# Performance work log

Hardware: AMD Instinct MI355X
Metric: run time of the kernel (lower is better)

Reference implementation:

```python
import jax, jax.numpy as jnp
import numpy as np

L_V, L_T, D, H, HID = 1024, 128, 4096, 8, 2048
N1 = L_V // 2      # tokens kept by selector module 1
N2 = N1 // 2       # tokens kept by selector module 2 (final selected)
N_REM = L_V - N2   # remaining tokens to merge


def setup_inputs() -> dict:
    key = jax.random.key(0)
    ks = jax.random.split(key, 8)
    s = 0.02
    return {
        "vision_feature": jax.random.normal(ks[0], (L_V, D), jnp.float32),
        "text_embed": jax.random.normal(ks[1], (L_T, D), jnp.float32),
        "attention_mask": jnp.ones((L_T,), jnp.int32),
        # stacked MHA params, order: [m1.global, m1.local, m2.global, m2.local]
        "attn_in_w": s * jax.random.normal(ks[2], (4, 3 * D, D), jnp.float32),
        "attn_in_b": jnp.zeros((4, 3 * D), jnp.float32),
        "attn_out_w": s * jax.random.normal(ks[3], (4, D, D), jnp.float32),
        "attn_out_b": jnp.zeros((4, D), jnp.float32),
        # stacked MLP params, order: [module1, module2]
        "mlp_w1": s * jax.random.normal(ks[4], (2, HID, D), jnp.float32),
        "mlp_b1": jnp.zeros((2, HID), jnp.float32),
        "mlp_w2": s * jax.random.normal(ks[5], (2, HID), jnp.float32),
        "mlp_b2": jnp.zeros((2,), jnp.float32),
    }


def _mha(xq, xkv, in_w, in_b, out_w, out_b):
    # torch nn.MultiheadAttention (unbatched, eval mode: no dropout)
    dh = D // H
    qw, kw, vw = jnp.split(in_w, 3, axis=0)
    qb, kb, vb = jnp.split(in_b, 3)
    q = (xq @ qw.T + qb).reshape(-1, H, dh)
    k = (xkv @ kw.T + kb).reshape(-1, H, dh)
    v = (xkv @ vw.T + vb).reshape(-1, H, dh)
    scores = jnp.einsum('qhd,khd->hqk', q, k) * (1.0 / np.sqrt(dh))
    attn = jax.nn.softmax(scores, axis=-1)
    o = jnp.einsum('hqk,khd->qhd', attn, v).reshape(-1, D)
    return o @ out_w.T + out_b


def _select(vf, te, pg, pl, w1, b1, w2, b2, n_keep):
    # TokenSelectionModule (deterministic top-k selection path, fixed shapes)
    comb = jnp.concatenate([vf, te], axis=0)
    g = _mha(vf, comb, *pg)
    l = _mha(vf, te, *pl) + vf
    x = jnp.stack([l, g], axis=1)                      # (L, 2, D): 0=local, 1=global
    h = jax.nn.relu(jnp.einsum('lcd,hd->lch', x, w1) + b1)
    logits = jnp.einsum('lch,h->lc', h, w2) + b2       # (L, 2)
    _, idx = jax.lax.top_k(logits[:, 1], n_keep)
    return vf[idx], idx


def _forward(vision_feature, text_embed, attn_in_w, attn_in_b, attn_out_w,
             attn_out_b, mlp_w1, mlp_b1, mlp_w2, mlp_b2):
    p = lambda i: (attn_in_w[i], attn_in_b[i], attn_out_w[i], attn_out_b[i])
    sv1, idx1 = _select(vision_feature, text_embed, p(0), p(1),
                        mlp_w1[0], mlp_b1[0], mlp_w2[0], mlp_b2[0], N1)
    sel, idx2 = _select(sv1, text_embed, p(2), p(3),
                        mlp_w1[1], mlp_b1[1], mlp_w2[1], mlp_b2[1], N2)
    sel_idx = idx1[idx2]

    # remaining = complement of selected indices (fixed size N_REM)
    sel_mask = jnp.zeros((L_V,), bool).at[sel_idx].set(True)
    rem_idx = jnp.nonzero(~sel_mask, size=N_REM)[0]
    rem = vision_feature[rem_idx]                      # (N_REM, D)

    # cosine similarity (torch eps=1e-8) + argmax matching
    nr = jnp.linalg.norm(rem, axis=-1)
    ns = jnp.linalg.norm(sel, axis=-1)
    sim = (rem @ sel.T) / jnp.maximum(nr[:, None] * ns[None, :], 1e-8)
    best = jnp.argmax(sim, axis=1)                     # (N_REM,) cluster ids

    # per-cluster gather+mean+normalize merge, vectorized as segment reduces
    cnt = jax.ops.segment_sum(jnp.ones((N_REM,), jnp.float32), best, num_segments=N2)
    sum_rem = jax.ops.segment_sum(rem, best, num_segments=N2)
    mean = (sel + sum_rem) / (cnt + 1.0)[:, None]
    seg_max = jax.ops.segment_max(nr, best, num_segments=N2)
    max_norm = jnp.maximum(ns, jnp.where(cnt > 0, seg_max, 0.0))
    mean_unit = mean / jnp.linalg.norm(mean, axis=-1, keepdims=True)
    updated = jnp.where((cnt > 0)[:, None], mean_unit * max_norm[:, None], sel)
    return updated  # top_k == 0 path: return merged selected features


def reference(vision_feature, text_embed, attention_mask, attn_in_w, attn_in_b,
              attn_out_w, attn_out_b, mlp_w1, mlp_b1, mlp_w2, mlp_b2):
    # attention_mask is accepted but unused, matching the torch forward
    return _forward(vision_feature, text_embed, attn_in_w, attn_in_b,
                    attn_out_w, attn_out_b, mlp_w1, mlp_b1, mlp_w2, mlp_b2)
```

## Files before the change

### kernel.cpp

```cpp
#include <hip/hip_runtime.h>
#include <hip/hip_bf16.h>
#include <math.h>
#include <stdint.h>

typedef __attribute__((ext_vector_type(4))) float f32x4;
typedef __attribute__((ext_vector_type(8))) short s16x8;
typedef __attribute__((ext_vector_type(4))) short s16x4;

struct sh2 { short hi, lo; };

__device__ __forceinline__ sh2 splitf(float x)
{
    __hip_bfloat16 h = __float2bfloat16(x);
    float hf = __bfloat162float(h);
    __hip_bfloat16 l = __float2bfloat16(x - hf);
    sh2 r;
    r.hi = __builtin_bit_cast(short, h);
    r.lo = __builtin_bit_cast(short, l);
    return r;
}

typedef const __attribute__((address_space(1))) void gvoid_t;
typedef __attribute__((address_space(3))) void lvoid_t;
__device__ __forceinline__ void gld_lds16(const void* g, void* l)
{
    __builtin_amdgcn_global_load_lds((gvoid_t*)(uintptr_t)g,
                                     (lvoid_t*)(uintptr_t)l, 16, 0, 0);
}

template<int BF, int EPI, bool RELU>
__global__ __launch_bounds__(256, 2) void mfma_gemm(
    const short* __restrict__ Ahi, const short* __restrict__ Alo, int lda, long sA,
    const float* __restrict__ Bf, const short* __restrict__ Bhi,
    const short* __restrict__ Blo, int ldb, long sB,
    float* __restrict__ Cf, short* __restrict__ Chi, short* __restrict__ Clo,
    short* __restrict__ Thi, short* __restrict__ Tlo, int ldc, int ldT, long sC,
    int K, int SK, float alpha, const float* __restrict__ bias)
{
    __shared__ short SH[2][16384];
    const int zf = blockIdx.z;
    const int sk = (SK > 1) ? (zf % SK) : 0;
    const int bz = (SK > 1) ? (zf / SK) : zf;
    const int Kc = K / SK;
    const int kb = sk * Kc;
    Ahi += (long)bz * sA; Alo += (long)bz * sA;
    if (BF == 0) Bf += (long)bz * sB; else { Bhi += (long)bz * sB; Blo += (long)bz * sB; }
    const long cofs = (long)((SK > 1) ? zf : bz) * sC;

    const int GX = gridDim.x, GY = gridDim.y;
    const int nwg = GX * GY;
    const int bid = blockIdx.x + GX * blockIdx.y;
    const int q8 = nwg >> 3, r8 = nwg & 7;
    const int xcd = bid & 7, sl = bid >> 3;
    const int t = (xcd < r8) ? (xcd * (q8 + 1) + sl)
                             : (r8 * (q8 + 1) + (xcd - r8) * q8 + sl);
    const int m0 = (t % GY) * 128, n0 = (t / GY) * 128;

    const int tid = threadIdx.x;
    const int lane = tid & 63, wave = tid >> 6;
    const int wr = (wave >> 1) * 64, wc = (wave & 1) * 64;
    const int lrow = lane & 15, lk = lane >> 4;
    const int cswz8 = (lk ^ ((lrow >> 1) & 3)) << 3;

    const int rA0 = wave * 16 + (lane >> 2);
    const int rA1 = rA0 + 64;
    const int sc0 = ((lane & 3) ^ ((rA0 >> 1) & 3)) * 8;
    const int sc1 = ((lane & 3) ^ ((rA1 >> 1) & 3)) * 8;
    const long gA0 = (long)(m0 + rA0) * lda + sc0;
    const long gA1 = (long)(m0 + rA1) * lda + sc1;
    long gB0 = 0, gB1 = 0;
    if (BF == 1) {
        gB0 = (long)(n0 + rA0) * ldb + sc0;
        gB1 = (long)(n0 + rA1) * ldb + sc1;
    }
    const int lw0 = wave * 512, lw1 = wave * 512 + 2048;

    const int brow = tid & 127;
    const int bkc0 = (tid >> 7) * 8;
    const int bkc1 = bkc0 + 16;
    const int bw0 = brow * 32 + (((bkc0 >> 3) ^ ((brow >> 1) & 3)) << 3);
    const int bw1 = brow * 32 + (((bkc1 >> 3) ^ ((brow >> 1) & 3)) << 3);
    const float* bpr = (BF == 0) ? Bf + (long)(n0 + brow) * ldb : nullptr;

    f32x4 acc[4][4];
#pragma unroll
    for (int i = 0; i < 4; i++)
#pragma unroll
        for (int j = 0; j < 4; j++) acc[i][j] = (f32x4){0.f, 0.f, 0.f, 0.f};

    float4 rb0a, rb0b, rb1a, rb1b;

    {
        short* S = &SH[0][0];
        gld_lds16(Ahi + gA0 + kb, S + lw0);
        gld_lds16(Ahi + gA1 + kb, S + lw1);
        gld_lds16(Alo + gA0 + kb, S + 4096 + lw0);
        gld_lds16(Alo + gA1 + kb, S + 4096 + lw1);
        if constexpr (BF == 1) {
            gld_lds16(Bhi + gB0 + kb, S + 8192 + lw0);
            gld_lds16(Bhi + gB1 + kb, S + 8192 + lw1);
            gld_lds16(Blo + gB0 + kb, S + 12288 + lw0);
            gld_lds16(Blo + gB1 + kb, S + 12288 + lw1);
        } else {
            rb0a = *(const float4*)(bpr + kb + bkc0);
            rb0b = *(const float4*)(bpr + kb + bkc0 + 4);
            rb1a = *(const float4*)(bpr + kb + bkc1);
            rb1b = *(const float4*)(bpr + kb + bkc1 + 4);
            s16x8 h, l; sh2 p;
            p = splitf(rb0a.x); h[0] = p.hi; l[0] = p.lo;
            p = splitf(rb0a.y); h[1] = p.hi; l[1] = p.lo;
            p = splitf(rb0a.z); h[2] = p.hi; l[2] = p.lo;
            p = splitf(rb0a.w); h[3] = p.hi; l[3] = p.lo;
            p = splitf(rb0b.x); h[4] = p.hi; l[4] = p.lo;
            p = splitf(rb0b.y); h[5] = p.hi; l[5] = p.lo;
            p = splitf(rb0b.z); h[6] = p.hi; l[6] = p.lo;
            p = splitf(rb0b.w); h[7] = p.hi; l[7] = p.lo;
            *(s16x8*)&S[8192 + bw0] = h;
            *(s16x8*)&S[12288 + bw0] = l;
            p = splitf(rb1a.x); h[0] = p.hi; l[0] = p.lo;
            p = splitf(rb1a.y); h[1] = p.hi; l[1] = p.lo;
            p = splitf(rb1a.z); h[2] = p.hi; l[2] = p.lo;
            p = splitf(rb1a.w); h[3] = p.hi; l[3] = p.lo;
            p = splitf(rb1b.x); h[4] = p.hi; l[4] = p.lo;
            p = splitf(rb1b.y); h[5] = p.hi; l[5] = p.lo;
            p = splitf(rb1b.z); h[6] = p.hi; l[6] = p.lo;
            p = splitf(rb1b.w); h[7] = p.hi; l[7] = p.lo;
            *(s16x8*)&S[8192 + bw1] = h;
            *(s16x8*)&S[12288 + bw1] = l;
        }
    }
    __syncthreads();

    int cur = 0;
    const int kend = kb + Kc;
    for (int k0 = kb; k0 < kend; k0 += 32) {
        const int kn = k0 + 32;
        const bool nx = (kn < kend);
        short* SN = &SH[cur ^ 1][0];
        if (nx) {
            gld_lds16(Ahi + gA0 + kn, SN + lw0);
            gld_lds16(Ahi + gA1 + kn, SN + lw1);
            gld_lds16(Alo + gA0 + kn, SN + 4096 + lw0);
            gld_lds16(Alo + gA1 + kn, SN + 4096 + lw1);
            if constexpr (BF == 1) {
                gld_lds16(Bhi + gB0 + kn, SN + 8192 + lw0);
                gld_lds16(Bhi + gB1 + kn, SN + 8192 + lw1);
                gld_lds16(Blo + gB0 + kn, SN + 12288 + lw0);
                gld_lds16(Blo + gB1 + kn, SN + 12288 + lw1);
            } else {
                rb0a = *(const float4*)(bpr + kn + bkc0);
                rb0b = *(const float4*)(bpr + kn + bkc0 + 4);
                rb1a = *(const float4*)(bpr + kn + bkc1);
                rb1b = *(const float4*)(bpr + kn + bkc1 + 4);
            }
        }
        const short* S = &SH[cur][0];
        s16x8 ah[4], al[4];
#pragma unroll
        for (int m = 0; m < 4; m++) {
            const int idx = (wr + m * 16 + lrow) * 32 + cswz8;
            ah[m] = *(const s16x8*)&S[idx];
            al[m] = *(const s16x8*)&S[4096 + idx];
        }
#pragma unroll
        for (int n = 0; n < 4; n++) {
            const int idx = (wc + n * 16 + lrow) * 32 + cswz8;
            const s16x8 bh = *(const s16x8*)&S[8192 + idx];
            const s16x8 bl = *(const s16x8*)&S[12288 + idx];
#pragma unroll
            for (int m = 0; m < 4; m++) {
                acc[m][n] = __builtin_amdgcn_mfma_f32_16x16x32_bf16(ah[m], bh, acc[m][n], 0, 0, 0);
                acc[m][n] = __builtin_amdgcn_mfma_f32_16x16x32_bf16(ah[m], bl, acc[m][n], 0, 0, 0);
                acc[m][n] = __builtin_amdgcn_mfma_f32_16x16x32_bf16(al[m], bh, acc[m][n], 0, 0, 0);
            }
        }
        if (BF == 0 && nx) {
            s16x8 h, l; sh2 p;
            p = splitf(rb0a.x); h[0] = p.hi; l[0] = p.lo;
            p = splitf(rb0a.y); h[1] = p.hi; l[1] = p.lo;
            p = splitf(rb0a.z); h[2] = p.hi; l[2] = p.lo;
            p = splitf(rb0a.w); h[3] = p.hi; l[3] = p.lo;
            p = splitf(rb0b.x); h[4] = p.hi; l[4] = p.lo;
            p = splitf(rb0b.y); h[5] = p.hi; l[5] = p.lo;
            p = splitf(rb0b.z); h[6] = p.hi; l[6] = p.lo;
            p = splitf(rb0b.w); h[7] = p.hi; l[7] = p.lo;
            *(s16x8*)&SN[8192 + bw0] = h;
            *(s16x8*)&SN[12288 + bw0] = l;
            p = splitf(rb1a.x); h[0] = p.hi; l[0] = p.lo;
            p = splitf(rb1a.y); h[1] = p.hi; l[1] = p.lo;
            p = splitf(rb1a.z); h[2] = p.hi; l[2] = p.lo;
            p = splitf(rb1a.w); h[3] = p.hi; l[3] = p.lo;
            p = splitf(rb1b.x); h[4] = p.hi; l[4] = p.lo;
            p = splitf(rb1b.y); h[5] = p.hi; l[5] = p.lo;
            p = splitf(rb1b.z); h[6] = p.hi; l[6] = p.lo;
            p = splitf(rb1b.w); h[7] = p.hi; l[7] = p.lo;
            *(s16x8*)&SN[8192 + bw1] = h;
            *(s16x8*)&SN[12288 + bw1] = l;
        }
        __syncthreads();
        cur ^= 1;
    }
#pragma unroll
    for (int n = 0; n < 4; n++) {
        const int col = n0 + wc + n * 16 + lrow;
        const float bv = (SK == 1 && bias) ? bias[col] : 0.f;
#pragma unroll
        for (int m = 0; m < 4; m++) {
            const int row = m0 + wr + m * 16 + lk * 4;
            if (SK > 1) {
#pragma unroll
                for (int r = 0; r < 4; r++)
                    Cf[cofs + (long)(row + r) * ldc + col] = acc[m][n][r] * alpha;
            } else if constexpr (EPI == 0) {
#pragma unroll
                for (int r = 0; r < 4; r++) {
                    float v = acc[m][n][r] * alpha + bv;
                    if (RELU) v = fmaxf(v, 0.f);
                    Cf[cofs + (long)(row + r) * ldc + col] = v;
                }
            } else if constexpr (EPI == 1) {
#pragma unroll
                for (int r = 0; r < 4; r++) {
                    float v = acc[m][n][r] * alpha + bv;
                    sh2 p = splitf(v);
                    Chi[cofs + (long)(row + r) * ldc + col] = p.hi;
                    Clo[cofs + (long)(row + r) * ldc + col] = p.lo;
                }
            } else {
                if (n0 < 8192) {
#pragma unroll
                    for (int r = 0; r < 4; r++) {
                        float v = acc[m][n][r] + bv;
                        sh2 p = splitf(v);
                        Chi[(long)(row + r) * ldc + col] = p.hi;
                        Clo[(long)(row + r) * ldc + col] = p.lo;
                    }
                } else {
                    s16x4 h4, l4;
#pragma unroll
                    for (int r = 0; r < 4; r++) {
                        float v = acc[m][n][r] + bv;
                        sh2 p = splitf(v);
                        h4[r] = p.hi; l4[r] = p.lo;
                    }
                    const long tof = (long)(col - 8192) * ldT + row;
                    *(s16x4*)&Thi[tof] = h4;
                    *(s16x4*)&Tlo[tof] = l4;
                }
            }
        }
    }
}

template<int EPI, bool RELU>
__global__ __launch_bounds__(256) void reduce_k(
    const float* __restrict__ P, long zstride, int SK, int total,
    int Ninner, int ldc, int colstep,
    float* __restrict__ Cf, short* __restrict__ Chi, short* __restrict__ Clo,
    const float* __restrict__ bias)
{
    const int bz = blockIdx.y;
    const long pbase = (long)bz * SK * zstride;
    const int e = (blockIdx.x * 256 + threadIdx.x) * 4;
    if (e >= total) return;
    const float* p = P + pbase + e;
    float4 s = *(const float4*)p;
    for (int k = 1; k < SK; k++) {
        float4 tv = *(const float4*)(p + (long)k * zstride);
        s.x += tv.x; s.y += tv.y; s.z += tv.z; s.w += tv.w;
    }
    const int r = e / Ninner, c = e % Ninner;
    const int col0 = colstep * bz + c;
    const long ob = (long)r * ldc + col0;
    float v[4] = {s.x, s.y, s.z, s.w};
#pragma unroll
    for (int j = 0; j < 4; j++) {
        float x = v[j] + (bias ? bias[col0 + j] : 0.f);
        if (RELU) x = fmaxf(x, 0.f);
        if constexpr (EPI == 0) {
            Cf[ob + j] = x;
        } else {
            sh2 pp = splitf(x);
            Chi[ob + j] = pp.hi;
            Clo[ob + j] = pp.lo;
        }
    }
}

__global__ __launch_bounds__(256) void split_rows(
    const float* __restrict__ src, const int* __restrict__ map,
    short* __restrict__ dhi, short* __restrict__ dlo)
{
    const int r = blockIdx.x;
    const int sr = map ? map[r] : r;
    const float4* s = (const float4*)(src + (long)sr * 4096);
    const long db = (long)r * 4096;
    for (int i = threadIdx.x; i < 1024; i += 256) {
        float4 f = s[i];
        s16x4 h, l;
        sh2 p;
        p = splitf(f.x); h[0] = p.hi; l[0] = p.lo;
        p = splitf(f.y); h[1] = p.hi; l[1] = p.lo;
        p = splitf(f.z); h[2] = p.hi; l[2] = p.lo;
        p = splitf(f.w); h[3] = p.hi; l[3] = p.lo;
        *(s16x4*)&dhi[db + i * 4] = h;
        *(s16x4*)&dlo[db + i * 4] = l;
    }
}

__global__ __launch_bounds__(256) void softmax_split(
    const float* __restrict__ x, short* __restrict__ phi, short* __restrict__ plo,
    int cols)
{
    const long rb = (long)blockIdx.x * cols;
    const float4* xr = (const float4*)(x + rb);
    const int t = threadIdx.x;
    const int n4 = cols >> 2;
    __shared__ float red[256];
    float mx = -INFINITY;
    for (int i = t; i < n4; i += 256) {
        float4 f = xr[i];
        mx = fmaxf(fmaxf(mx, fmaxf(f.x, f.y)), fmaxf(f.z, f.w));
    }
    red[t] = mx; __syncthreads();
    for (int off = 128; off; off >>= 1) { if (t < off) red[t] = fmaxf(red[t], red[t + off]); __syncthreads(); }
    mx = red[0]; __syncthreads();
    float4 ebuf[2];
    float s = 0.f;
    int nb = 0;
    for (int i = t; i < n4; i += 256) {
        float4 f = xr[i];
        f.x = expf(f.x - mx); f.y = expf(f.y - mx); f.z = expf(f.z - mx); f.w = expf(f.w - mx);
        ebuf[nb++] = f;
        s += f.x + f.y + f.z + f.w;
    }
    red[t] = s; __syncthreads();
    for (int off = 128; off; off >>= 1) { if (t < off) red[t] += red[t + off]; __syncthreads(); }
    s = red[0];
    nb = 0;
    for (int i = t; i < n4; i += 256) {
        float4 f = ebuf[nb++];
        f.x /= s; f.y /= s; f.z /= s; f.w /= s;
        s16x4 h, l;
        sh2 p;
        p = splitf(f.x); h[0] = p.hi; l[0] = p.lo;
        p = splitf(f.y); h[1] = p.hi; l[1] = p.lo;
        p = splitf(f.z); h[2] = p.hi; l[2] = p.lo;
        p = splitf(f.w); h[3] = p.hi; l[3] = p.lo;
        *(s16x4*)&phi[rb + i * 4] = h;
        *(s16x4*)&plo[rb + i * 4] = l;
    }
}

__global__ __launch_bounds__(256) void gemv_kernel(
    const float* __restrict__ H, const float* __restrict__ w2,
    const float* __restrict__ b2, float* __restrict__ logits)
{
    const int r = blockIdx.x, t = threadIdx.x;
    const float* row = H + (long)r * 2048;
    float s = 0.f;
    for (int c = t; c < 2048; c += 256) s += row[c] * w2[c];
    __shared__ float red[256];
    red[t] = s; __syncthreads();
    for (int off = 128; off; off >>= 1) { if (t < off) red[t] += red[t + off]; __syncthreads(); }
    if (!t) logits[r] = red[0] + b2[0];
}

__global__ void topk_kernel(const float* __restrict__ vals, int n, int k, int* __restrict__ out)
{
    __shared__ float sv[1024];
    __shared__ int   si[1024];
    const int t = threadIdx.x;
    sv[t] = vals[t]; si[t] = t;
    for (int size = 2; size <= n; size <<= 1) {
        for (int stride = size >> 1; stride > 0; stride >>= 1) {
            __syncthreads();
            const int j = t ^ stride;
            if (j > t) {
                float av = sv[t], bv = sv[j];
                int ai = si[t], bi = si[j];
                const bool before = (av > bv) || (av == bv && ai < bi);
                const bool dir = ((t & size) == 0);
                if (dir ? !before : before) { sv[t] = bv; si[t] = bi; sv[j] = av; si[j] = ai; }
            }
        }
    }
    __syncthreads();
    if (t < k) out[t] = si[t];
}

__global__ void gather_sel_kernel(const int* __restrict__ idx1, const int* __restrict__ idx2,
                                  int* __restrict__ selidx)
{
    const int t = threadIdx.x;
    if (t < 256) selidx[t] = idx1[idx2[t]];
}

__global__ void complement_kernel(const int* __restrict__ selidx, int* __restrict__ remidx)
{
    __shared__ int mask[1024];
    __shared__ int scan[1024];
    const int t = threadIdx.x;
    mask[t] = 0;
    __syncthreads();
    if (t < 256) mask[selidx[t]] = 1;
    __syncthreads();
    const int keep = 1 - mask[t];
    scan[t] = keep;
    __syncthreads();
    for (int off = 1; off < 1024; off <<= 1) {
        int v = scan[t];
        if (t >= off) v += scan[t - off];
        __syncthreads();
        scan[t] = v;
        __syncthreads();
    }
    if (keep) remidx[scan[t] - 1] = t;
}

__global__ __launch_bounds__(256) void gather_rows_kernel(
    float* __restrict__ dst, const float* __restrict__ src,
    const int* __restrict__ map, int ncols)
{
    const int r = blockIdx.x;
    const int sr = map[r];
    const float4* s = (const float4*)(src + (long)sr * ncols);
    float4* d = (float4*)(dst + (long)r * ncols);
    for (int i = threadIdx.x; i < ncols / 4; i += 256) d[i] = s[i];
}

__global__ __launch_bounds__(256) void rownorm_kernel(
    const float* __restrict__ x, float* __restrict__ out)
{
    const int r = blockIdx.x, t = threadIdx.x;
    const float* row = x + (long)r * 4096;
    float s = 0.f;
    for (int c = t; c < 4096; c += 256) { float v = row[c]; s += v * v; }
    __shared__ float red[256];
    red[t] = s; __syncthreads();
    for (int off = 128; off; off >>= 1) { if (t < off) red[t] += red[t + off]; __syncthreads(); }
    if (!t) out[r] = sqrtf(red[0]);
}

__global__ __launch_bounds__(256) void argmax_kernel(
    const float* __restrict__ S, const float* __restrict__ nr,
    const float* __restrict__ ns, int* __restrict__ best)
{
    const int r = blockIdx.x, t = threadIdx.x;
    float v = S[(long)r * 256 + t] / fmaxf(nr[r] * ns[t], 1e-8f);
    __shared__ float bv[256];
    __shared__ int bi[256];
    bv[t] = v; bi[t] = t; __syncthreads();
    for (int off = 128; off; off >>= 1) {
        if (t < off) {
            float ov = bv[t + off]; int oi = bi[t + off];
            if (ov > bv[t] || (ov == bv[t] && oi < bi[t])) { bv[t] = ov; bi[t] = oi; }
        }
        __syncthreads();
    }
    if (!t) best[r] = bi[0];
}

__global__ __launch_bounds__(256) void merge_kernel(
    const float* __restrict__ selb, const float* __restrict__ rem,
    const int* __restrict__ best, const float* __restrict__ nr,
    const float* __restrict__ ns, float* __restrict__ out)
{
    const int j = blockIdx.x, t = threadIdx.x;
    __shared__ int sbest[768];
    __shared__ float snr[768];
    __shared__ float red[256];
    for (int i = t; i < 768; i += 256) { sbest[i] = best[i]; snr[i] = nr[i]; }
    __syncthreads();
    float acc[16];
#pragma unroll
    for (int d = 0; d < 16; d++) acc[d] = 0.f;
    int cnt = 0; float smax = 0.f;
    const int base = t * 16;
    for (int i = 0; i < 768; i++) {
        if (sbest[i] == j) {
            cnt++;
            smax = fmaxf(smax, snr[i]);
            const float* rp = rem + (long)i * 4096 + base;
#pragma unroll
            for (int d = 0; d < 16; d += 4) {
                float4 x4 = *(const float4*)(rp + d);
                acc[d] += x4.x; acc[d + 1] += x4.y; acc[d + 2] += x4.z; acc[d + 3] += x4.w;
            }
        }
    }
    const float* sp = selb + (long)j * 4096 + base;
    float mean[16]; float ss = 0.f;
    const float denom = (float)(cnt + 1);
#pragma unroll
    for (int d = 0; d < 16; d++) { mean[d] = (sp[d] + acc[d]) / denom; ss += mean[d] * mean[d]; }
    red[t] = ss; __syncthreads();
    for (int off = 128; off; off >>= 1) { if (t < off) red[t] += red[t + off]; __syncthreads(); }
    const float nm = sqrtf(red[0]);
    const float mx = fmaxf(ns[j], cnt > 0 ? smax : 0.f);
    float* op = out + (long)j * 4096 + base;
#pragma unroll
    for (int d = 0; d < 16; d++) op[d] = (cnt > 0) ? (mean[d] / nm) * mx : sp[d];
}

extern "C" void kernel_launch(void* const* d_in, const int* in_sizes, int n_in,
                              void* d_out, int out_size, void* d_ws, size_t ws_size,
                              hipStream_t stream)
{
    const float* vf   = (const float*)d_in[0];
    const float* te   = (const float*)d_in[1];
    const float* inw  = (const float*)d_in[3];
    const float* inb  = (const float*)d_in[4];
    const float* outw = (const float*)d_in[5];
    const float* outb = (const float*)d_in[6];
    const float* w1   = (const float*)d_in[7];
    const float* b1   = (const float*)d_in[8];
    const float* w2   = (const float*)d_in[9];
    const float* b2   = (const float*)d_in[10];
    float* out = (float*)d_out;
    char* base = (char*)d_ws;

    char* qkR = base;
    char* vTR = base + 37748736;
    char* scR = vTR + 18874368;
    float* smalls = (float*)(scR + 37748736);

    short* qkhi = (short*)qkR;
    short* qklo = (short*)(qkR + 18874368);
    short* vThi = (short*)vTR;
    short* vTlo = (short*)(vTR + 9437184);
    float* hbuf = (float*)scR;

    float* logits = smalls;
    float* nr     = smalls + 1024;
    float* ns     = smalls + 1792;
    int* idx1   = (int*)(smalls + 2048);
    int* idx2   = (int*)(smalls + 2560);
    int* selidx = (int*)(smalls + 2816);
    int* remidx = (int*)(smalls + 3072);
    int* best   = (int*)(smalls + 3840);

    const float scl = (float)(1.0 / sqrt(512.0));

    for (int m = 0; m < 2; m++) {
        const int Mq  = m ? 512 : 1024;
        const int Mkv = m ? 640 : 1152;
        const float* Wqkv = inw + (size_t)(2 * m) * 12288 * 4096;
        const float* bqkv = inb + (size_t)(2 * m) * 12288;
        const float* ow = outw + (size_t)(2 * m) * 4096 * 4096;
        const float* ob = outb + (size_t)(2 * m) * 4096;

        short* chi = (short*)scR;
        short* clo = (short*)(scR + (size_t)Mkv * 4096 * 2);
        if (m == 0) {
            split_rows<<<1024, 256, 0, stream>>>(vf, nullptr, chi, clo);
            split_rows<<<128, 256, 0, stream>>>(te, nullptr,
                chi + (size_t)1024 * 4096, clo + (size_t)1024 * 4096);
        } else {
            split_rows<<<512, 256, 0, stream>>>(vf, idx1, chi, clo);
            split_rows<<<128, 256, 0, stream>>>(te, nullptr,
                chi + (size_t)512 * 4096, clo + (size_t)512 * 4096);
        }
        mfma_gemm<0, 2, false><<<dim3(96, Mkv / 128, 1), 256, 0, stream>>>(
            chi, clo, 4096, 0, Wqkv, nullptr, nullptr, 4096, 0,
            nullptr, qkhi, qklo, vThi, vTlo, 8192, 1152, 0, 4096, 1, 1.f, bqkv);
        float* scor = (float*)(m ? (scR + 10485760) : scR);
        mfma_gemm<1, 0, false><<<dim3(Mkv / 128, Mq / 128, 8), 256, 0, stream>>>(
            qkhi, qklo, 8192, 512, nullptr, qkhi + 4096, qklo + 4096, 8192, 512,
            scor, nullptr, nullptr, nullptr, nullptr, Mkv, 0, (long)Mq * Mkv,
            512, 1, scl, nullptr);
        short* phi = (short*)qkR;
        short* plo = (short*)(qkR + (size_t)8 * Mq * Mkv * 2);
        softmax_split<<<8 * Mq, 256, 0, stream>>>(scor, phi, plo, Mkv);
        short* ohi = (short*)scR;
        short* olo = (short*)(scR + (size_t)Mq * 4096 * 2);
        if (m == 0) {
            mfma_gemm<1, 1, false><<<dim3(4, 8, 8), 256, 0, stream>>>(
                phi, plo, Mkv, (long)Mq * Mkv, nullptr, vThi, vTlo, 1152, 512L * 1152,
                nullptr, ohi, olo, nullptr, nullptr, 4096, 0, 512, Mkv, 1, 1.f, nullptr);
        } else {
            float* Ppv = (float*)(qkR + 20971520);
            mfma_gemm<1, 0, false><<<dim3(4, 4, 16), 256, 0, stream>>>(
                phi, plo, Mkv, (long)Mq * Mkv, nullptr, vThi, vTlo, 1152, 512L * 1152,
                Ppv, nullptr, nullptr, nullptr, nullptr, 512, 0, 262144,
                Mkv, 2, 1.f, nullptr);
            reduce_k<1, false><<<dim3(256, 8), 256, 0, stream>>>(
                Ppv, 262144, 2, 262144, 512, 4096, 512, nullptr, ohi, olo, nullptr);
        }
        short* ghi = (short*)(scR + (size_t)Mq * 4096 * 4);
        short* glo = (short*)(scR + (size_t)Mq * 4096 * 6);
        {
            float* Pg = (float*)qkR;
            const long zst = (long)Mq * 4096;
            mfma_gemm<0, 0, false><<<dim3(32, Mq / 128, 2), 256, 0, stream>>>(
                ohi, olo, 4096, 0, ow, nullptr, nullptr, 4096, 0,
                Pg, nullptr, nullptr, nullptr, nullptr, 4096, 0, zst,
                4096, 2, 1.f, nullptr);
            reduce_k<1, false><<<dim3((int)(zst / 1024), 1), 256, 0, stream>>>(
                Pg, zst, 2, (int)zst, 4096, 4096, 0, nullptr, ghi, glo, ob);
        }
        {
            float* Pm = (float*)(qkR + 8388608);
            const long zst = (long)Mq * 2048;
            mfma_gemm<0, 0, false><<<dim3(16, Mq / 128, 4), 256, 0, stream>>>(
                ghi, glo, 4096, 0, w1 + (size_t)m * 2048 * 4096, nullptr, nullptr, 4096, 0,
                Pm, nullptr, nullptr, nullptr, nullptr, 2048, 0, zst,
                4096, 4, 1.f, nullptr);
            reduce_k<0, true><<<dim3((int)(zst / 1024), 1), 256, 0, stream>>>(
                Pm, zst, 4, (int)zst, 2048, 2048, 0, hbuf, nullptr, nullptr,
                b1 + (size_t)m * 2048);
        }
        gemv_kernel<<<Mq, 256, 0, stream>>>(hbuf, w2 + (size_t)m * 2048, b2 + m, logits);
        if (m == 0) topk_kernel<<<1, 1024, 0, stream>>>(logits, 1024, 512, idx1);
        else        topk_kernel<<<1, 512, 0, stream>>>(logits, 512, 256, idx2);
    }

    short* remhi = (short*)scR;
    short* remlo = (short*)(scR + 6291456);
    short* selhi = (short*)(scR + 12582912);
    short* sello = (short*)(scR + 14680064);
    float* rem_f = (float*)(scR + 16777216);
    float* sel_f = (float*)(scR + 29360128);
    float* Smat  = (float*)(scR + 33554432);

    gather_sel_kernel<<<1, 256, 0, stream>>>(idx1, idx2, selidx);
    complement_kernel<<<1, 1024, 0, stream>>>(selidx, remidx);
    split_rows<<<768, 256, 0, stream>>>(vf, remidx, remhi, remlo);
    split_rows<<<256, 256, 0, stream>>>(vf, selidx, selhi, sello);
    gather_rows_kernel<<<768, 256, 0, stream>>>(rem_f, vf, remidx, 4096);
    gather_rows_kernel<<<256, 256, 0, stream>>>(sel_f, vf, selidx, 4096);
    rownorm_kernel<<<768, 256, 0, stream>>>(rem_f, nr);
    rownorm_kernel<<<256, 256, 0, stream>>>(sel_f, ns);
    {
        float* Ps = (float*)qkR;
        mfma_gemm<1, 0, false><<<dim3(2, 6, 8), 256, 0, stream>>>(
            remhi, remlo, 4096, 0, nullptr, selhi, sello, 4096, 0,
            Ps, nullptr, nullptr, nullptr, nullptr, 256, 0, 196608,
            4096, 8, 1.f, nullptr);
        reduce_k<0, false><<<dim3(192, 1), 256, 0, stream>>>(
            Ps, 196608, 8, 196608, 256, 256, 0, Smat, nullptr, nullptr, nullptr);
    }
    argmax_kernel<<<768, 256, 0, stream>>>(Smat, nr, ns, best);
    merge_kernel<<<256, 256, 0, stream>>>(sel_f, rem_f, best, nr, ns, out);
}
```

Measured before the change: 1.399 ms.

## Use 256x256-tile QKV projection GEMM for module one with XCD-aware block mapping

Adds a 512-thread GEMM kernel with 256x256 output tiles and uses it for the first module's fused QKV projection. Larger M tiles cut how many times the fp32 weight matrix is streamed and split from global memory. It also remaps block ids across XCDs for locality. The cost is padding rows beyond 1152, out-of-range A reads, fewer blocks and higher register and LDS pressure.

Result: faster. 1.301 ms (-7.0%).

```diff
diff --git a/kernel.cpp b/kernel.cpp
--- a/kernel.cpp
+++ b/kernel.cpp
@@ -18,6 +18,20 @@
     r.hi = __builtin_bit_cast(short, h);
     r.lo = __builtin_bit_cast(short, l);
     return r;
+}
+
+__device__ __forceinline__ void split8(const float4& a, const float4& b,
+                                       s16x8& h, s16x8& l)
+{
+    sh2 p;
+    p = splitf(a.x); h[0] = p.hi; l[0] = p.lo;
+    p = splitf(a.y); h[1] = p.hi; l[1] = p.lo;
+    p = splitf(a.z); h[2] = p.hi; l[2] = p.lo;
+    p = splitf(a.w); h[3] = p.hi; l[3] = p.lo;
+    p = splitf(b.x); h[4] = p.hi; l[4] = p.lo;
+    p = splitf(b.y); h[5] = p.hi; l[5] = p.lo;
+    p = splitf(b.z); h[6] = p.hi; l[6] = p.lo;
+    p = splitf(b.w); h[7] = p.hi; l[7] = p.lo;
 }
 
 typedef const __attribute__((address_space(1))) void gvoid_t;
@@ -106,25 +120,11 @@
             rb0b = *(const float4*)(bpr + kb + bkc0 + 4);
             rb1a = *(const float4*)(bpr + kb + bkc1);
             rb1b = *(const float4*)(bpr + kb + bkc1 + 4);
-            s16x8 h, l; sh2 p;
-            p = splitf(rb0a.x); h[0] = p.hi; l[0] = p.lo;
-            p = splitf(rb0a.y); h[1] = p.hi; l[1] = p.lo;
-            p = splitf(rb0a.z); h[2] = p.hi; l[2] = p.lo;
-            p = splitf(rb0a.w); h[3] = p.hi; l[3] = p.lo;
-            p = splitf(rb0b.x); h[4] = p.hi; l[4] = p.lo;
-            p = splitf(rb0b.y); h[5] = p.hi; l[5] = p.lo;
-            p = splitf(rb0b.z); h[6] = p.hi; l[6] = p.lo;
-            p = splitf(rb0b.w); h[7] = p.hi; l[7] = p.lo;
+            s16x8 h, l;
+            split8(rb0a, rb0b, h, l);
             *(s16x8*)&S[8192 + bw0] = h;
             *(s16x8*)&S[12288 + bw0] = l;
-            p = splitf(rb1a.x); h[0] = p.hi; l[0] = p.lo;
-            p = splitf(rb1a.y); h[1] = p.hi; l[1] = p.lo;
-            p = splitf(rb1a.z); h[2] = p.hi; l[2] = p.lo;
-            p = splitf(rb1a.w); h[3] = p.hi; l[3] = p.lo;
-            p = splitf(rb1b.x); h[4] = p.hi; l[4] = p.lo;
-            p = splitf(rb1b.y); h[5] = p.hi; l[5] = p.lo;
-            p = splitf(rb1b.z); h[6] = p.hi; l[6] = p.lo;
-            p = splitf(rb1b.w); h[7] = p.hi; l[7] = p.lo;
+            split8(rb1a, rb1b, h, l);
             *(s16x8*)&S[8192 + bw1] = h;
             *(s16x8*)&S[12288 + bw1] = l;
         }
@@ -175,25 +175,11 @@
             }
         }
         if (BF == 0 && nx) {
-            s16x8 h, l; sh2 p;
-            p = splitf(rb0a.x); h[0] = p.hi; l[0] = p.lo;
-            p = splitf(rb0a.y); h[1] = p.hi; l[1] = p.lo;
-            p = splitf(rb0a.z); h[2] = p.hi; l[2] = p.lo;
-            p = splitf(rb0a.w); h[3] = p.hi; l[3] = p.lo;
-            p = splitf(rb0b.x); h[4] = p.hi; l[4] = p.lo;
-            p = splitf(rb0b.y); h[5] = p.hi; l[5] = p.lo;
-            p = splitf(rb0b.z); h[6] = p.hi; l[6] = p.lo;
-            p = splitf(rb0b.w); h[7] = p.hi; l[7] = p.lo;
+            s16x8 h, l;
+            split8(rb0a, rb0b, h, l);
             *(s16x8*)&SN[8192 + bw0] = h;
             *(s16x8*)&SN[12288 + bw0] = l;
-            p = splitf(rb1a.x); h[0] = p.hi; l[0] = p.lo;
-            p = splitf(rb1a.y); h[1] = p.hi; l[1] = p.lo;
-            p = splitf(rb1a.z); h[2] = p.hi; l[2] = p.lo;
-            p = splitf(rb1a.w); h[3] = p.hi; l[3] = p.lo;
-            p = splitf(rb1b.x); h[4] = p.hi; l[4] = p.lo;
-            p = splitf(rb1b.y); h[5] = p.hi; l[5] = p.lo;
-            p = splitf(rb1b.z); h[6] = p.hi; l[6] = p.lo;
-            p = splitf(rb1b.w); h[7] = p.hi; l[7] = p.lo;
+            split8(rb1a, rb1b, h, l);
             *(s16x8*)&SN[8192 + bw1] = h;
             *(s16x8*)&SN[12288 + bw1] = l;
         }
@@ -227,6 +213,152 @@
                     Clo[cofs + (long)(row + r) * ldc + col] = p.lo;
                 }
             } else {
+                if (n0 < 8192) {
+#pragma unroll
+                    for (int r = 0; r < 4; r++) {
+                        float v = acc[m][n][r] + bv;
+                        sh2 p = splitf(v);
+                        Chi[(long)(row + r) * ldc + col] = p.hi;
+                        Clo[(long)(row + r) * ldc + col] = p.lo;
+                    }
+                } else {
+                    s16x4 h4, l4;
+#pragma unroll
+                    for (int r = 0; r < 4; r++) {
+                        float v = acc[m][n][r] + bv;
+                        sh2 p = splitf(v);
+                        h4[r] = p.hi; l4[r] = p.lo;
+                    }
+                    const long tof = (long)(col - 8192) * ldT + row;
+                    *(s16x4*)&Thi[tof] = h4;
+                    *(s16x4*)&Tlo[tof] = l4;
+                }
+            }
+        }
+    }
+}
+
+__global__ __launch_bounds__(512, 2) void mfma_gemm256(
+    const short* __restrict__ Ahi, const short* __restrict__ Alo, int lda,
+    const float* __restrict__ Bf, int ldb,
+    short* __restrict__ Chi, short* __restrict__ Clo,
+    short* __restrict__ Thi, short* __restrict__ Tlo, int ldc, int ldT,
+    int K, int Mreal, const float* __restrict__ bias)
+{
+    __shared__ short SH[2][32768];
+
+    const int GX = gridDim.x, GY = gridDim.y;
+    const int nwg = GX * GY;
+    const int bid = blockIdx.x + GX * blockIdx.y;
+    const int q8 = nwg >> 3, r8 = nwg & 7;
+    const int xcd = bid & 7, sl = bid >> 3;
+    const int t = (xcd < r8) ? (xcd * (q8 + 1) + sl)
+                             : (r8 * (q8 + 1) + (xcd - r8) * q8 + sl);
+    const int m0 = (t % GY) * 256, n0 = (t / GY) * 256;
+
+    const int tid = threadIdx.x;
+    const int lane = tid & 63, wave = tid >> 6;
+    const int wr = (wave >> 1) * 64, wc = (wave & 1) * 128;
+    const int lrow = lane & 15, lk = lane >> 4;
+    const int cswz8 = (lk ^ ((lrow >> 1) & 3)) << 3;
+
+    const int rA0 = wave * 32 + (lane >> 2);
+    const int rA1 = rA0 + 16;
+    const int sc0 = ((lane & 3) ^ ((rA0 >> 1) & 3)) * 8;
+    const int sc1 = ((lane & 3) ^ ((rA1 >> 1) & 3)) * 8;
+    const long gA0 = (long)(m0 + rA0) * lda + sc0;
+    const long gA1 = (long)(m0 + rA1) * lda + sc1;
+    const int lw0 = wave * 1024, lw1 = wave * 1024 + 512;
+
+    const int brow = tid & 255;
+    const int bk = (tid >> 8) * 16;
+    const int bw0 = brow * 32 + ((((bk >> 3) + 0) ^ ((brow >> 1) & 3)) << 3);
+    const int bw1 = brow * 32 + ((((bk >> 3) + 1) ^ ((brow >> 1) & 3)) << 3);
+    const float* bpr = Bf + (long)(n0 + brow) * ldb + bk;
+
+    f32x4 acc[4][8];
+#pragma unroll
+    for (int i = 0; i < 4; i++)
+#pragma unroll
+        for (int j = 0; j < 8; j++) acc[i][j] = (f32x4){0.f, 0.f, 0.f, 0.f};
+
+    float4 rb0, rb1, rb2, rb3;
+
+    {
+        short* S = &SH[0][0];
+        gld_lds16(Ahi + gA0, S + lw0);
+        gld_lds16(Ahi + gA1, S + lw1);
+        gld_lds16(Alo + gA0, S + 8192 + lw0);
+        gld_lds16(Alo + gA1, S + 8192 + lw1);
+        rb0 = *(const float4*)(bpr + 0);
+        rb1 = *(const float4*)(bpr + 4);
+        rb2 = *(const float4*)(bpr + 8);
+        rb3 = *(const float4*)(bpr + 12);
+        s16x8 h, l;
+        split8(rb0, rb1, h, l);
+        *(s16x8*)&S[16384 + bw0] = h;
+        *(s16x8*)&S[24576 + bw0] = l;
+        split8(rb2, rb3, h, l);
+        *(s16x8*)&S[16384 + bw1] = h;
+        *(s16x8*)&S[24576 + bw1] = l;
+    }
+    __syncthreads();
+
+    int cur = 0;
+    for (int k0 = 0; k0 < K; k0 += 32) {
+        const int kn = k0 + 32;
+        const bool nx = (kn < K);
+        short* SN = &SH[cur ^ 1][0];
+        if (nx) {
+            gld_lds16(Ahi + gA0 + kn, SN + lw0);
+            gld_lds16(Ahi + gA1 + kn, SN + lw1);
+            gld_lds16(Alo + gA0 + kn, SN + 8192 + lw0);
+            gld_lds16(Alo + gA1 + kn, SN + 8192 + lw1);
+            rb0 = *(const float4*)(bpr + kn + 0);
+            rb1 = *(const float4*)(bpr + kn + 4);
+            rb2 = *(const float4*)(bpr + kn + 8);
+            rb3 = *(const float4*)(bpr + kn + 12);
+        }
+        const short* S = &SH[cur][0];
+        s16x8 ah[4], al[4];
+#pragma unroll
+        for (int m = 0; m < 4; m++) {
+            const int idx = (wr + m * 16 + lrow) * 32 + cswz8;
+            ah[m] = *(const s16x8*)&S[idx];
+            al[m] = *(const s16x8*)&S[8192 + idx];
+        }
+#pragma unroll
+        for (int n = 0; n < 8; n++) {
+            const int idx = (wc + n * 16 + lrow) * 32 + cswz8;
+            const s16x8 bh = *(const s16x8*)&S[16384 + idx];
+            const s16x8 bl = *(const s16x8*)&S[24576 + idx];
+#pragma unroll
+            for (int m = 0; m < 4; m++) {
+                acc[m][n] = __builtin_amdgcn_mfma_f32_16x16x32_bf16(ah[m], bh, acc[m][n], 0, 0, 0);
+                acc[m][n] = __builtin_amdgcn_mfma_f32_16x16x32_bf16(ah[m], bl, acc[m][n], 0, 0, 0);
+                acc[m][n] = __builtin_amdgcn_mfma_f32_16x16x32_bf16(al[m], bh, acc[m][n], 0, 0, 0);
+            }
+        }
+        if (nx) {
+            s16x8 h, l;
+            split8(rb0, rb1, h, l);
+            *(s16x8*)&SN[16384 + bw0] = h;
+            *(s16x8*)&SN[24576 + bw0] = l;
+            split8(rb2, rb3, h, l);
+            *(s16x8*)&SN[16384 + bw1] = h;
+            *(s16x8*)&SN[24576 + bw1] = l;
+        }
+        __syncthreads();
+        cur ^= 1;
+    }
+#pragma unroll
+    for (int n = 0; n < 8; n++) {
+        const int col = n0 + wc + n * 16 + lrow;
+        const float bv = bias[col];
+#pragma unroll
+        for (int m = 0; m < 4; m++) {
+            const int row = m0 + wr + m * 16 + lk * 4;
+            if (row < Mreal) {
                 if (n0 < 8192) {
 #pragma unroll
                     for (int r = 0; r < 4; r++) {
@@ -561,9 +693,15 @@
             split_rows<<<128, 256, 0, stream>>>(te, nullptr,
                 chi + (size_t)512 * 4096, clo + (size_t)512 * 4096);
         }
-        mfma_gemm<0, 2, false><<<dim3(96, Mkv / 128, 1), 256, 0, stream>>>(
-            chi, clo, 4096, 0, Wqkv, nullptr, nullptr, 4096, 0,
-            nullptr, qkhi, qklo, vThi, vTlo, 8192, 1152, 0, 4096, 1, 1.f, bqkv);
+        if (m == 0) {
+            mfma_gemm256<<<dim3(48, 5, 1), 512, 0, stream>>>(
+                chi, clo, 4096, Wqkv, 4096, qkhi, qklo, vThi, vTlo,
+                8192, 1152, 4096, 1152, bqkv);
+        } else {
+            mfma_gemm<0, 2, false><<<dim3(96, Mkv / 128, 1), 256, 0, stream>>>(
+                chi, clo, 4096, 0, Wqkv, nullptr, nullptr, 4096, 0,
+                nullptr, qkhi, qklo, vThi, vTlo, 8192, 1152, 0, 4096, 1, 1.f, bqkv);
+        }
         float* scor = (float*)(m ? (scR + 10485760) : scR);
         mfma_gemm<1, 0, false><<<dim3(Mkv / 128, Mq / 128, 8), 256, 0, stream>>>(
             qkhi, qklo, 8192, 512, nullptr, qkhi + 4096, qklo + 4096, 8192, 512,
```
